# Optimization experiments

Measured on AMD Instinct MI355X. Metric: run time of the kernel, lower is better.

## Reference

```python
import jax, jax.numpy as jnp
import numpy as np

B, N, C, H = 4, 1024, 1024, 16
HD = C // H  # 64
THETA = 10000.0


def _rope_cos_sin(n, hd, theta):
    # classic 1D RoPE cache; [n, hd] with each freq repeated twice (interleaved pairs)
    inv_freq = 1.0 / theta ** (jnp.arange(0, hd, 2, dtype=jnp.float32) / hd)
    t = jnp.arange(n, dtype=jnp.float32)
    freqs = t[:, None] * inv_freq[None, :]              # [n, hd/2]
    cos = jnp.repeat(jnp.cos(freqs), 2, axis=-1)        # [n, hd]
    sin = jnp.repeat(jnp.sin(freqs), 2, axis=-1)
    # original clones & forces row 0 to identity rotation (already true since t=0)
    cos = cos.at[0].set(1.0)
    sin = sin.at[0].set(0.0)
    return cos, sin


def _rotate_half(x):
    # interleaved rotate-half: (x0,x1,x2,x3,...) -> (-x1,x0,-x3,x2,...)
    x1 = x[..., 0::2]
    x2 = x[..., 1::2]
    return jnp.stack((-x2, x1), axis=-1).reshape(x.shape)


def setup_inputs() -> dict:
    key = jax.random.key(0)
    ks = jax.random.split(key, 5)
    s = 0.02
    return {
        "x": jax.random.normal(ks[0], (B, N, C), dtype=jnp.float32),
        "qkv_w": jax.random.normal(ks[1], (3 * C, C), dtype=jnp.float32) * s,
        "qkv_b": jax.random.normal(ks[2], (3 * C,), dtype=jnp.float32) * s,
        "proj_w": jax.random.normal(ks[3], (C, C), dtype=jnp.float32) * s,
        "proj_b": jax.random.normal(ks[4], (C,), dtype=jnp.float32) * s,
    }


def reference(x, qkv_w, qkv_b, proj_w, proj_b):
    b, n, c = x.shape
    h, hd = H, HD
    qkv = x @ qkv_w.T + qkv_b                              # [b, n, 3c]
    qkv = qkv.reshape(b, n, 3, h, hd).transpose(2, 0, 3, 1, 4)  # [3, b, h, n, hd]
    q, k, v = qkv[0], qkv[1], qkv[2]
    scale = hd ** -0.5
    q = q * scale                                          # explicit pre-scale (as in source)
    cos, sin = _rope_cos_sin(n, hd, THETA)                 # [n, hd]
    cos = cos[None, None]                                  # broadcast over b, h
    sin = sin[None, None]
    q = q * cos + _rotate_half(q) * sin
    k = k * cos + _rotate_half(k) * sin
    # F.scaled_dot_product_attention also applies its default 1/sqrt(hd) scale
    logits = jnp.einsum('bhqd,bhkd->bhqk', q, k) * scale   # [b, h, n, n]
    attn = jax.nn.softmax(logits, axis=-1)
    out = jnp.einsum('bhqk,bhkd->bhqd', attn, v)           # [b, h, n, hd]
    out = out.transpose(0, 2, 1, 3).reshape(b, n, c)
    return out @ proj_w.T + proj_b
```

## Files before the change

### kernel.cpp

```cpp
#include <hip/hip_runtime.h>
#include <hip/hip_bf16.h>
#include <stdint.h>

#define DEVI __device__ __forceinline__

typedef __attribute__((ext_vector_type(8))) short short8;
typedef __attribute__((ext_vector_type(4))) short short4v;
typedef __attribute__((ext_vector_type(4))) float floatx4;

DEVI ushort f2bf(float f) {
  union { float f; uint32_t u; } v; v.f = f;
  uint32_t u = v.u;
  uint32_t r = (u + 0x7FFFu + ((u >> 16) & 1u)) >> 16;
  return (ushort)r;
}
DEVI ushort f2bf_fast(float f) {
  union { float f; uint32_t u; } v; v.f = f;
  return (ushort)((v.u + 0x8000u) >> 16);
}
DEVI float bf2f(ushort h) {
  union { uint32_t u; float f; } v; v.u = ((uint32_t)h) << 16;
  return v.f;
}
DEVI void gld_lds16(const void* g, void* l) {
  __builtin_amdgcn_global_load_lds(
      (const __attribute__((address_space(1))) unsigned int*)g,
      (__attribute__((address_space(3))) unsigned int*)l, 16, 0, 0);
}

__global__ __launch_bounds__(256, 4) void cast_all(
    const float* __restrict__ x, const float* __restrict__ w1,
    const float* __restrict__ w2, ushort* __restrict__ xb,
    ushort* __restrict__ w1b, ushort* __restrict__ w2b) {
  const int N1 = 4096 * 1024, N2 = 3072 * 1024, N3 = 1024 * 1024;
  int i = (blockIdx.x * 256 + threadIdx.x) * 4;
  const int total = N1 + N2 + N3;
  int stride = gridDim.x * 256 * 4;
  for (; i < total; i += stride) {
    const float* src; ushort* dst; int off;
    if (i < N1) { src = x; dst = xb; off = i; }
    else if (i < N1 + N2) { src = w1; dst = w1b; off = i - N1; }
    else { src = w2; dst = w2b; off = i - N1 - N2; }
    float4 v = *(const float4*)(src + off);
    ushort4 o;
    o.x = f2bf(v.x); o.y = f2bf(v.y); o.z = f2bf(v.z); o.w = f2bf(v.w);
    *(ushort4*)(dst + off) = o;
  }
}

__global__ __launch_bounds__(256, 4) void rope_table(float2* __restrict__ tab) {
  int id = blockIdx.x * 256 + threadIdx.x;
  int j = id & 31, n = id >> 5;
  float inv = powf(10000.0f, -(float)(2 * j) / 64.0f);
  float fr = (float)n * inv;
  tab[id] = make_float2(cosf(fr), sinf(fr));
}

__global__ __launch_bounds__(256, 4) void gemm_qkv(
    const ushort* __restrict__ A, const ushort* __restrict__ Bm,
    const float* __restrict__ bias, const float2* __restrict__ tab,
    ushort* __restrict__ Qb, ushort* __restrict__ Kb,
    ushort* __restrict__ Vsrc) {
  __shared__ __align__(16) char As[2][8192];
  __shared__ __align__(16) char Bs[2][8192];
  const int tid = threadIdx.x;
  const int w = tid >> 6, lane = tid & 63;

  const int bid = blockIdx.x;
  const int xcd = bid & 7, i5 = bid >> 3;
  const int lm = i5 & 7, ln = i5 >> 3;
  const int mt = (xcd & 3) * 8 + lm;
  const int nt = (xcd >> 2) * 12 + ln;
  const int m0 = mt * 128, n0 = nt * 128;

  const int wm = (w >> 1) * 64, wn = (w & 1) * 64;
  const int lrow = lane & 15, g = lane >> 4;
  const int swrd = (g ^ ((lrow >> 1) & 3)) << 4;

  const int swsrc = (((lane & 3) ^ ((lane >> 3) & 3)) << 4);
  const char* aG = (const char*)A + (size_t)(m0 + w * 32 + (lane >> 2)) * 2048 + swsrc;
  const char* bG = (const char*)Bm + (size_t)(n0 + w * 32 + (lane >> 2)) * 2048 + swsrc;
  const int ldst = w * 2048 + lane * 16;

  auto STAGE = [&](const int buf) {
    gld_lds16(aG, &As[buf][0] + ldst);
    gld_lds16(aG + 16 * 2048, &As[buf][0] + ldst + 1024);
    gld_lds16(bG, &Bs[buf][0] + ldst);
    gld_lds16(bG + 16 * 2048, &Bs[buf][0] + ldst + 1024);
    aG += 64; bG += 64;
  };

  floatx4 acc[4][4] = {};

  auto TILE = [&](const int buf) {
    short8 af[4], bf[4];
#pragma unroll
    for (int t = 0; t < 4; ++t) {
      af[t] = *(const short8*)(&As[buf][0] + (wm + t * 16 + lrow) * 64 + swrd);
      bf[t] = *(const short8*)(&Bs[buf][0] + (wn + t * 16 + lrow) * 64 + swrd);
    }
#pragma unroll
    for (int i = 0; i < 4; ++i)
#pragma unroll
      for (int j = 0; j < 4; ++j)
        acc[i][j] = __builtin_amdgcn_mfma_f32_16x16x32_bf16(af[i], bf[j], acc[i][j], 0, 0, 0);
  };

  STAGE(0);
  asm volatile("s_waitcnt vmcnt(0)" ::: "memory");
  __builtin_amdgcn_s_barrier();
  __builtin_amdgcn_sched_barrier(0);

  for (int t = 0; t < 32; t += 2) {
    STAGE(1);
    __builtin_amdgcn_sched_barrier(0);
    TILE(0);
    asm volatile("s_waitcnt vmcnt(0)" ::: "memory");
    __builtin_amdgcn_s_barrier();
    __builtin_amdgcn_sched_barrier(0);

    if (t + 2 < 32) STAGE(0);
    __builtin_amdgcn_sched_barrier(0);
    TILE(1);
    asm volatile("s_waitcnt vmcnt(0)" ::: "memory");
    __builtin_amdgcn_s_barrier();
    __builtin_amdgcn_sched_barrier(0);
  }

  const int role = n0 >> 10;
  const float sc = (1.0f / 64.0f) * 1.44269504088896f;
#pragma unroll
  for (int i = 0; i < 4; ++i) {
    int mrow = m0 + wm + i * 16 + (lane >> 4) * 4;
#pragma unroll
    for (int j = 0; j < 4; ++j) {
      int ncol = n0 + wn + j * 16 + (lane & 15);
      float bv = bias[ncol];
      int cm = ncol & 1023;
      int h = cm >> 6, d = cm & 63;
#pragma unroll
      for (int r = 0; r < 4; ++r) {
        float v = acc[i][j][r] + bv;
        int row = mrow + r;
        int b = row >> 10, n = row & 1023;
        if (role == 2) {
          Vsrc[(size_t)row * 1024 + cm] = f2bf(v);
        } else {
          float p = __shfl_xor(v, 1);
          float2 cs = tab[n * 32 + (d >> 1)];
          float o = (d & 1) ? (v * cs.x + p * cs.y) : (v * cs.x - p * cs.y);
          if (role == 0) o *= sc;
          ushort* dst = (role == 0) ? Qb : Kb;
          dst[((size_t)(b * 16 + h) * 1024 + n) * 64 + d] = f2bf(o);
        }
      }
    }
  }
}

__global__ __launch_bounds__(256, 3) void gemm_proj(
    const ushort* __restrict__ A, const ushort* __restrict__ Bm,
    const float* __restrict__ bias, float* __restrict__ Cout) {
  const int K = 1024;
  __shared__ char lds[3][16384];
  char* L0 = &lds[0][0];
  const int tid = threadIdx.x;
  const int w = tid >> 6, lane = tid & 63;

  const int bid = blockIdx.x;
  const int xcd = bid & 7, i5 = bid >> 3;
  const int lm = i5 & 7, ln = i5 >> 3;
  const int mt = (xcd & 3) * 8 + lm;
  const int nt = (xcd >> 2) * 4 + ln;
  const int m0 = mt * 128, n0 = nt * 128;

  const int wm = (w >> 1) * 64, wn = (w & 1) * 64;
  const int lrow = lane & 15, lk2 = (lane >> 4) * 16;

  const ushort* agp = A + (size_t)(m0 + w * 32 + (lane >> 2)) * K + (lane & 3) * 8;
  const ushort* bgp = Bm + (size_t)(n0 + w * 32 + (lane >> 2)) * K + (lane & 3) * 8;
  const int stoff = w * 2048 + lane * 16;

  auto STAGE = [&](const int base) {
    char* L = L0 + base;
    gld_lds16(agp, L + stoff);
    gld_lds16(agp + 16 * K, L + stoff + 1024);
    gld_lds16(bgp, L + 8192 + stoff);
    gld_lds16(bgp + 16 * K, L + 8192 + stoff + 1024);
    agp += 32; bgp += 32;
  };

  floatx4 acc[4][4] = {};

  auto TILE = [&](const int base) {
    const char* L = L0 + base;
    short8 af[4], bf[4];
#pragma unroll
    for (int t = 0; t < 4; ++t) {
      af[t] = *(const short8*)(L + (wm + t * 16 + lrow) * 64 + lk2);
      bf[t] = *(const short8*)(L + 8192 + (wn + t * 16 + lrow) * 64 + lk2);
    }
#pragma unroll
    for (int i = 0; i < 4; ++i)
#pragma unroll
      for (int j = 0; j < 4; ++j)
        acc[i][j] = __builtin_amdgcn_mfma_f32_16x16x32_bf16(af[i], bf[j], acc[i][j], 0, 0, 0);
  };

  STAGE(0);
  STAGE(16384);
  int bT = 0, bS = 32768;

  for (int t = 0; t < 31; ++t) {
    asm volatile("s_waitcnt vmcnt(4)" ::: "memory");
    __builtin_amdgcn_s_barrier();
    __builtin_amdgcn_sched_barrier(0);
    if (t < 30) STAGE(bS);
    __builtin_amdgcn_sched_barrier(0);
    TILE(bT);
    __builtin_amdgcn_sched_barrier(0);
    bT += 16384; if (bT == 49152) bT = 0;
    bS += 16384; if (bS == 49152) bS = 0;
  }
  asm volatile("s_waitcnt vmcnt(0)" ::: "memory");
  __builtin_amdgcn_s_barrier();
  __builtin_amdgcn_sched_barrier(0);
  TILE(bT);

#pragma unroll
  for (int i = 0; i < 4; ++i) {
    int mrow = m0 + wm + i * 16 + (lane >> 4) * 4;
#pragma unroll
    for (int j = 0; j < 4; ++j) {
      int ncol = n0 + wn + j * 16 + (lane & 15);
      float bv = bias[ncol];
#pragma unroll
      for (int r = 0; r < 4; ++r)
        Cout[(size_t)(mrow + r) * 1024 + ncol] = acc[i][j][r] + bv;
    }
  }
}

__global__ __launch_bounds__(256, 4) void v_trans(
    const ushort* __restrict__ Vsrc, ushort* __restrict__ Vt) {
  __shared__ ushort t[64][72];
  int bh = blockIdx.y, ntile = blockIdx.x;
  int b = bh >> 4, h = bh & 15;
  int n0 = ntile * 64;
  int tid = threadIdx.x;
  int r = tid >> 2, cc = (tid & 3) * 16;
  const ushort* src = Vsrc + (size_t)(b * 1024 + n0 + r) * 1024 + h * 64 + cc;
  *(short8*)(&t[r][cc]) = *(const short8*)(src);
  *(short8*)(&t[r][cc + 8]) = *(const short8*)(src + 8);
  __syncthreads();
  int d = tid >> 2;
  ushort outv[16];
#pragma unroll
  for (int i = 0; i < 16; ++i) outv[i] = t[cc + i][d];
  ushort* dst = Vt + (size_t)bh * 65536 + (size_t)d * 1024 + n0 + cc;
  *(short8*)(dst) = *(const short8*)(outv);
  *(short8*)(dst + 8) = *(const short8*)(outv + 8);
}

__global__ __launch_bounds__(256, 4) void attn(
    const ushort* __restrict__ Q, const ushort* __restrict__ Kc,
    const ushort* __restrict__ Vt, ushort* __restrict__ AO) {
  __shared__ char lds[2][16384];
  char* ldsbase = &lds[0][0];
  int id = blockIdx.x;
  int bh = id & 63, qi = id >> 6;
  int b = bh >> 4, h = bh & 15;
  int q0 = qi * 64;
  int tid = threadIdx.x, w = tid >> 6, lane = tid & 63;
  int l15 = lane & 15, g = lane >> 4;
  const ushort* Qbh = Q + (size_t)bh * 65536;
  const char* Kbh = (const char*)(Kc + (size_t)bh * 65536);
  const char* Vbh = (const char*)(Vt + (size_t)bh * 65536);

  short8 qf[2];
#pragma unroll
  for (int ks = 0; ks < 2; ++ks)
    qf[ks] = *(const short8*)(Qbh + (size_t)(q0 + w * 16 + l15) * 64 + ks * 32 + g * 8);

  int kaddr[8];
#pragma unroll
  for (int ks = 0; ks < 2; ++ks)
#pragma unroll
    for (int nt = 0; nt < 4; ++nt) {
      int row = nt * 16 + l15;
      kaddr[ks * 4 + nt] = (row * 128 + ks * 64 + g * 16) ^ ((row & 7) << 4);
    }
  int vaddr[16];
#pragma unroll
  for (int ch = 0; ch < 2; ++ch)
#pragma unroll
    for (int dt = 0; dt < 4; ++dt)
#pragma unroll
      for (int hf = 0; hf < 2; ++hf) {
        int row = dt * 16 + l15;
        vaddr[(ch * 4 + dt) * 2 + hf] =
            8192 + ((row * 128 + ch * 64 + hf * 32 + g * 8) ^ ((row & 7) << 4));
      }

  const int d0 = w * 2048 + lane * 16;
  const int d1 = d0 + 1024;
  const int r0 = d0 >> 7, r1 = d1 >> 7;
  const int s0 = d0 ^ ((r0 & 7) << 4), s1 = d1 ^ ((r1 & 7) << 4);
  const char* pK0 = Kbh + s0;
  const char* pK1 = Kbh + s1;
  const char* pV0 = Vbh + r0 * 2048 + (s0 & 127);
  const char* pV1 = Vbh + r1 * 2048 + (s1 & 127);

  auto STAGE = [&](const int B) {
    gld_lds16(pK0, ldsbase + B + d0);
    gld_lds16(pK1, ldsbase + B + d1);
    gld_lds16(pV0, ldsbase + B + 8192 + d0);
    gld_lds16(pV1, ldsbase + B + 8192 + d1);
    pK0 += 8192; pK1 += 8192; pV0 += 128; pV1 += 128;
  };

  floatx4 oacc[4] = {};
  float lrun = 0.f;

  auto TILE = [&](const int B) {
    floatx4 sacc[4] = {};
    __builtin_amdgcn_s_setprio(1);
#pragma unroll
    for (int ks = 0; ks < 2; ++ks) {
      short8 kf[4];
#pragma unroll
      for (int nt = 0; nt < 4; ++nt)
        kf[nt] = *(const short8*)(ldsbase + B + kaddr[ks * 4 + nt]);
#pragma unroll
      for (int nt = 0; nt < 4; ++nt)
        sacc[nt] = __builtin_amdgcn_mfma_f32_16x16x32_bf16(kf[nt], qf[ks], sacc[nt], 0, 0, 0);
    }
    __builtin_amdgcn_s_setprio(0);

    float rs = 0.f;
#pragma unroll
    for (int nt = 0; nt < 4; ++nt)
#pragma unroll
      for (int r = 0; r < 4; ++r) {
        float p = __builtin_amdgcn_exp2f(sacc[nt][r]);
        sacc[nt][r] = p;
        rs += p;
      }
    lrun += rs;

    short8 pa[2];
#pragma unroll
    for (int ch = 0; ch < 2; ++ch)
#pragma unroll
      for (int r = 0; r < 4; ++r) {
        pa[ch][r] = (short)f2bf_fast(sacc[2 * ch][r]);
        pa[ch][r + 4] = (short)f2bf_fast(sacc[2 * ch + 1][r]);
      }

    __builtin_amdgcn_s_setprio(1);
#pragma unroll
    for (int ch = 0; ch < 2; ++ch)
#pragma unroll
      for (int dt = 0; dt < 4; ++dt) {
        short4v va = *(const short4v*)(ldsbase + B + vaddr[(ch * 4 + dt) * 2]);
        short4v vb = *(const short4v*)(ldsbase + B + vaddr[(ch * 4 + dt) * 2 + 1]);
        short8 vf = __builtin_shufflevector(va, vb, 0, 1, 2, 3, 4, 5, 6, 7);
        oacc[dt] = __builtin_amdgcn_mfma_f32_16x16x32_bf16(pa[ch], vf, oacc[dt], 0, 0, 0);
      }
    __builtin_amdgcn_s_setprio(0);
  };

  STAGE(0);
  asm volatile("s_waitcnt vmcnt(0)" ::: "memory");
  __builtin_amdgcn_s_barrier();
  __builtin_amdgcn_sched_barrier(0);

  for (int kt = 0; kt < 16; kt += 2) {
    STAGE(16384);
    __builtin_amdgcn_sched_barrier(0);
    TILE(0);
    asm volatile("s_waitcnt vmcnt(0)" ::: "memory");
    __builtin_amdgcn_s_barrier();
    __builtin_amdgcn_sched_barrier(0);

    if (kt + 2 < 16) STAGE(0);
    __builtin_amdgcn_sched_barrier(0);
    TILE(16384);
    asm volatile("s_waitcnt vmcnt(0)" ::: "memory");
    __builtin_amdgcn_s_barrier();
    __builtin_amdgcn_sched_barrier(0);
  }

  lrun += __shfl_xor(lrun, 16);
  lrun += __shfl_xor(lrun, 32);
  float linv = 1.0f / lrun;
  float linvR[4];
#pragma unroll
  for (int r = 0; r < 4; ++r) linvR[r] = __shfl(linv, g * 4 + r);
#pragma unroll
  for (int r = 0; r < 4; ++r) {
    int nseq = q0 + w * 16 + g * 4 + r;
#pragma unroll
    for (int dt = 0; dt < 4; ++dt) {
      int d = dt * 16 + l15;
      AO[(size_t)(b * 1024 + nseq) * 1024 + h * 64 + d] = f2bf(oacc[dt][r] * linvR[r]);
    }
  }
}

extern "C" void kernel_launch(void* const* d_in, const int* in_sizes, int n_in,
                              void* d_out, int out_size, void* d_ws, size_t ws_size,
                              hipStream_t stream) {
  const float* x = (const float*)d_in[0];
  const float* qkv_w = (const float*)d_in[1];
  const float* qkv_b = (const float*)d_in[2];
  const float* proj_w = (const float*)d_in[3];
  const float* proj_b = (const float*)d_in[4];
  float* out = (float*)d_out;

  char* ws = (char*)d_ws;
  size_t off = 0;
  auto alloc = [&](size_t bytes) -> void* {
    void* p = ws + off;
    off += (bytes + 255) & ~(size_t)255;
    return p;
  };
  ushort* xb = (ushort*)alloc(4096ull * 1024 * 2);
  ushort* wqkvb = (ushort*)alloc(3072ull * 1024 * 2);
  ushort* wprojb = (ushort*)alloc(1024ull * 1024 * 2);
  ushort* Qb = (ushort*)alloc(64ull * 1024 * 64 * 2);
  ushort* Kb = (ushort*)alloc(64ull * 1024 * 64 * 2);
  ushort* Vsrc = (ushort*)alloc(4096ull * 1024 * 2);
  ushort* Vt = (ushort*)alloc(64ull * 1024 * 64 * 2);
  ushort* AO = (ushort*)alloc(4096ull * 1024 * 2);
  float2* tab = (float2*)alloc(1024ull * 32 * sizeof(float2));

  cast_all<<<2048, 256, 0, stream>>>(x, qkv_w, proj_w, xb, wqkvb, wprojb);
  rope_table<<<128, 256, 0, stream>>>(tab);

  gemm_qkv<<<768, 256, 0, stream>>>(xb, wqkvb, qkv_b, tab, Qb, Kb, Vsrc);

  dim3 gv(16, 64);
  v_trans<<<gv, 256, 0, stream>>>(Vsrc, Vt);

  attn<<<1024, 256, 0, stream>>>(Qb, Kb, Vt, AO);

  gemm_proj<<<256, 256, 0, stream>>>(AO, wprojb, proj_b, out);
}
```

Baseline: 104.7 us.

## Widen QKV GEMM tile to 128x256, fuse RoPE table into cast, swizzle proj LDS

The QKV GEMM now computes 128x256 output tiles with 384 blocks: each wave holds a 64x128 accumulator and the B tile in LDS doubles. This raises operand reuse per LDS read but increases register pressure, and occupancy drops to 2 blocks per CU. The RoPE table computation is folded into the cast kernel, removing one launch. The projection GEMM adopts the same XOR-swizzled LDS layout as the QKV GEMM to cut bank conflicts.

```diff
diff --git a/kernel.cpp b/kernel.cpp
--- a/kernel.cpp
+++ b/kernel.cpp
@@ -31,9 +31,17 @@
 __global__ __launch_bounds__(256, 4) void cast_all(
     const float* __restrict__ x, const float* __restrict__ w1,
     const float* __restrict__ w2, ushort* __restrict__ xb,
-    ushort* __restrict__ w1b, ushort* __restrict__ w2b) {
+    ushort* __restrict__ w1b, ushort* __restrict__ w2b,
+    float2* __restrict__ tab) {
   const int N1 = 4096 * 1024, N2 = 3072 * 1024, N3 = 1024 * 1024;
-  int i = (blockIdx.x * 256 + threadIdx.x) * 4;
+  int id = blockIdx.x * 256 + threadIdx.x;
+  if (id < 32768) {
+    int j = id & 31, n = id >> 5;
+    float inv = powf(10000.0f, -(float)(2 * j) / 64.0f);
+    float fr = (float)n * inv;
+    tab[id] = make_float2(cosf(fr), sinf(fr));
+  }
+  int i = id * 4;
   const int total = N1 + N2 + N3;
   int stride = gridDim.x * 256 * 4;
   for (; i < total; i += stride) {
@@ -48,61 +56,56 @@
   }
 }
 
-__global__ __launch_bounds__(256, 4) void rope_table(float2* __restrict__ tab) {
-  int id = blockIdx.x * 256 + threadIdx.x;
-  int j = id & 31, n = id >> 5;
-  float inv = powf(10000.0f, -(float)(2 * j) / 64.0f);
-  float fr = (float)n * inv;
-  tab[id] = make_float2(cosf(fr), sinf(fr));
-}
-
-__global__ __launch_bounds__(256, 4) void gemm_qkv(
+__global__ __launch_bounds__(256, 2) void gemm_qkv(
     const ushort* __restrict__ A, const ushort* __restrict__ Bm,
     const float* __restrict__ bias, const float2* __restrict__ tab,
     ushort* __restrict__ Qb, ushort* __restrict__ Kb,
     ushort* __restrict__ Vsrc) {
   __shared__ __align__(16) char As[2][8192];
-  __shared__ __align__(16) char Bs[2][8192];
+  __shared__ __align__(16) char Bs[2][16384];
   const int tid = threadIdx.x;
   const int w = tid >> 6, lane = tid & 63;
 
   const int bid = blockIdx.x;
-  const int xcd = bid & 7, i5 = bid >> 3;
-  const int lm = i5 & 7, ln = i5 >> 3;
+  const int xcd = bid & 7, loc = bid >> 3;
+  const int lm = loc & 7, ln = loc >> 3;
   const int mt = (xcd & 3) * 8 + lm;
-  const int nt = (xcd >> 2) * 12 + ln;
-  const int m0 = mt * 128, n0 = nt * 128;
-
-  const int wm = (w >> 1) * 64, wn = (w & 1) * 64;
+  const int ntile = (xcd >> 2) * 6 + ln;
+  const int m0 = mt * 128, n0 = ntile * 256;
+
+  const int wm = (w >> 1) * 64, wn = (w & 1) * 128;
   const int lrow = lane & 15, g = lane >> 4;
   const int swrd = (g ^ ((lrow >> 1) & 3)) << 4;
 
   const int swsrc = (((lane & 3) ^ ((lane >> 3) & 3)) << 4);
   const char* aG = (const char*)A + (size_t)(m0 + w * 32 + (lane >> 2)) * 2048 + swsrc;
-  const char* bG = (const char*)Bm + (size_t)(n0 + w * 32 + (lane >> 2)) * 2048 + swsrc;
-  const int ldst = w * 2048 + lane * 16;
+  const char* bG = (const char*)Bm + (size_t)(n0 + w * 64 + (lane >> 2)) * 2048 + swsrc;
+  const int ldstA = w * 2048 + lane * 16;
+  const int ldstB = w * 4096 + lane * 16;
 
   auto STAGE = [&](const int buf) {
-    gld_lds16(aG, &As[buf][0] + ldst);
-    gld_lds16(aG + 16 * 2048, &As[buf][0] + ldst + 1024);
-    gld_lds16(bG, &Bs[buf][0] + ldst);
-    gld_lds16(bG + 16 * 2048, &Bs[buf][0] + ldst + 1024);
+    gld_lds16(aG, &As[buf][0] + ldstA);
+    gld_lds16(aG + 16 * 2048, &As[buf][0] + ldstA + 1024);
+#pragma unroll
+    for (int t = 0; t < 4; ++t)
+      gld_lds16(bG + (size_t)t * 16 * 2048, &Bs[buf][0] + ldstB + t * 1024);
     aG += 64; bG += 64;
   };
 
-  floatx4 acc[4][4] = {};
+  floatx4 acc[4][8] = {};
 
   auto TILE = [&](const int buf) {
-    short8 af[4], bf[4];
-#pragma unroll
-    for (int t = 0; t < 4; ++t) {
+    short8 af[4], bf[8];
+#pragma unroll
+    for (int t = 0; t < 4; ++t)
       af[t] = *(const short8*)(&As[buf][0] + (wm + t * 16 + lrow) * 64 + swrd);
-      bf[t] = *(const short8*)(&Bs[buf][0] + (wn + t * 16 + lrow) * 64 + swrd);
-    }
+#pragma unroll
+    for (int j = 0; j < 8; ++j)
+      bf[j] = *(const short8*)(&Bs[buf][0] + (wn + j * 16 + lrow) * 64 + swrd);
 #pragma unroll
     for (int i = 0; i < 4; ++i)
 #pragma unroll
-      for (int j = 0; j < 4; ++j)
+      for (int j = 0; j < 8; ++j)
         acc[i][j] = __builtin_amdgcn_mfma_f32_16x16x32_bf16(af[i], bf[j], acc[i][j], 0, 0, 0);
   };
 
@@ -133,7 +136,7 @@
   for (int i = 0; i < 4; ++i) {
     int mrow = m0 + wm + i * 16 + (lane >> 4) * 4;
 #pragma unroll
-    for (int j = 0; j < 4; ++j) {
+    for (int j = 0; j < 8; ++j) {
       int ncol = n0 + wn + j * 16 + (lane & 15);
       float bv = bias[ncol];
       int cm = ncol & 1023;
@@ -161,8 +164,7 @@
 __global__ __launch_bounds__(256, 3) void gemm_proj(
     const ushort* __restrict__ A, const ushort* __restrict__ Bm,
     const float* __restrict__ bias, float* __restrict__ Cout) {
-  const int K = 1024;
-  __shared__ char lds[3][16384];
+  __shared__ __align__(16) char lds[3][16384];
   char* L0 = &lds[0][0];
   const int tid = threadIdx.x;
   const int w = tid >> 6, lane = tid & 63;
@@ -175,19 +177,21 @@
   const int m0 = mt * 128, n0 = nt * 128;
 
   const int wm = (w >> 1) * 64, wn = (w & 1) * 64;
-  const int lrow = lane & 15, lk2 = (lane >> 4) * 16;
-
-  const ushort* agp = A + (size_t)(m0 + w * 32 + (lane >> 2)) * K + (lane & 3) * 8;
-  const ushort* bgp = Bm + (size_t)(n0 + w * 32 + (lane >> 2)) * K + (lane & 3) * 8;
-  const int stoff = w * 2048 + lane * 16;
+  const int lrow = lane & 15, g = lane >> 4;
+  const int swrd = (g ^ ((lrow >> 1) & 3)) << 4;
+
+  const int swsrc = (((lane & 3) ^ ((lane >> 3) & 3)) << 4);
+  const char* aG = (const char*)A + (size_t)(m0 + w * 32 + (lane >> 2)) * 2048 + swsrc;
+  const char* bG = (const char*)Bm + (size_t)(n0 + w * 32 + (lane >> 2)) * 2048 + swsrc;
+  const int ldst = w * 2048 + lane * 16;
 
   auto STAGE = [&](const int base) {
     char* L = L0 + base;
-    gld_lds16(agp, L + stoff);
-    gld_lds16(agp + 16 * K, L + stoff + 1024);
-    gld_lds16(bgp, L + 8192 + stoff);
-    gld_lds16(bgp + 16 * K, L + 8192 + stoff + 1024);
-    agp += 32; bgp += 32;
+    gld_lds16(aG, L + ldst);
+    gld_lds16(aG + 16 * 2048, L + ldst + 1024);
+    gld_lds16(bG, L + 8192 + ldst);
+    gld_lds16(bG + 16 * 2048, L + 8192 + ldst + 1024);
+    aG += 64; bG += 64;
   };
 
   floatx4 acc[4][4] = {};
@@ -197,8 +201,8 @@
     short8 af[4], bf[4];
 #pragma unroll
     for (int t = 0; t < 4; ++t) {
-      af[t] = *(const short8*)(L + (wm + t * 16 + lrow) * 64 + lk2);
-      bf[t] = *(const short8*)(L + 8192 + (wn + t * 16 + lrow) * 64 + lk2);
+      af[t] = *(const short8*)(L + (wm + t * 16 + lrow) * 64 + swrd);
+      bf[t] = *(const short8*)(L + 8192 + (wn + t * 16 + lrow) * 64 + swrd);
     }
 #pragma unroll
     for (int i = 0; i < 4; ++i)
@@ -435,10 +439,9 @@
   ushort* AO = (ushort*)alloc(4096ull * 1024 * 2);
   float2* tab = (float2*)alloc(1024ull * 32 * sizeof(float2));
 
-  cast_all<<<2048, 256, 0, stream>>>(x, qkv_w, proj_w, xb, wqkvb, wprojb);
-  rope_table<<<128, 256, 0, stream>>>(tab);
-
-  gemm_qkv<<<768, 256, 0, stream>>>(xb, wqkvb, qkv_b, tab, Qb, Kb, Vsrc);
+  cast_all<<<2048, 256, 0, stream>>>(x, qkv_w, proj_w, xb, wqkvb, wprojb, tab);
+
+  gemm_qkv<<<384, 256, 0, stream>>>(xb, wqkvb, qkv_b, tab, Qb, Kb, Vsrc);
 
   dim3 gv(16, 64);
   v_trans<<<gv, 256, 0, stream>>>(Vsrc, Vt);
```

Result: slower. 112.6 us (+7.6%).
